# Kernel optimization log

Hardware: AMD Instinct MI355X
Metric: run time of the kernel (lower is better)

Reference implementation:

```python
import jax, jax.numpy as jnp
import numpy as np

N = 50000        # nodes
E = 800000       # edges (avg degree 16)
HIDDEN = 256
HEADS = 8
HEAD_DIM = HIDDEN // HEADS


def _linear_params(key, fan_in, fan_out):
    k1, k2 = jax.random.split(key)
    s = 1.0 / np.sqrt(fan_in)
    W = jax.random.uniform(k1, (fan_in, fan_out), jnp.float32, -s, s)
    b = jax.random.uniform(k2, (fan_out,), jnp.float32, -s, s)
    return W, b


def setup_inputs() -> dict:
    key = jax.random.key(0)
    ks = jax.random.split(key, 7)
    h = jax.random.normal(ks[0], (N, HIDDEN), jnp.float32)
    # sparse adjacency nonzeros: row = destination node, col = source node
    row = jnp.sort(jax.random.randint(ks[1], (E,), 0, N))
    col = jax.random.randint(ks[2], (E,), 0, N)
    Wq, bq = _linear_params(ks[3], HIDDEN, HIDDEN)
    Wk, bk = _linear_params(ks[4], HIDDEN, HIDDEN)
    Wv, bv = _linear_params(ks[5], HIDDEN, HIDDEN)
    Wo, bo = _linear_params(ks[6], HIDDEN, HIDDEN)
    return dict(h=h, row=row, col=col, Wq=Wq, bq=bq, Wk=Wk, bk=bk,
                Wv=Wv, bv=bv, Wo=Wo, bo=bo)


def reference(h, row, col, Wq, bq, Wk, bk, Wv, bv, Wo, bo):
    n = h.shape[0]
    scaling = HEAD_DIM ** (-0.5)
    q = ((h @ Wq + bq).reshape(n, HEADS, HEAD_DIM)) * scaling
    k = (h @ Wk + bk).reshape(n, HEADS, HEAD_DIM)
    v = (h @ Wv + bv).reshape(n, HEADS, HEAD_DIM)

    # bsddmm: per-edge, per-head sampled dot product q[dst] . k[src] -> [E, H]
    s = jnp.einsum('ehd,ehd->eh', q[row], k[col])

    # sparse row-wise softmax over each destination node's incoming edges
    m = jax.ops.segment_max(s, row, num_segments=n)          # [N, H]
    p = jnp.exp(s - m[row])                                   # [E, H]
    denom = jax.ops.segment_sum(p, row, num_segments=n)      # [N, H]
    attn = p / denom[row]                                     # [E, H]

    # bspmm: out[dst] = sum over incoming edges attn * v[src] -> [N, H, D]
    out = jax.ops.segment_sum(attn[:, :, None] * v[col], row, num_segments=n)
    return out.reshape(n, HIDDEN) @ Wo + bo
```

## Files before the change

kernel.cpp:

```cpp
#include <hip/hip_runtime.h>
#include <math.h>


typedef __attribute__((ext_vector_type(8))) short bf16x8;
typedef __attribute__((ext_vector_type(4))) float f32x4;
typedef __attribute__((ext_vector_type(2))) float f32x2;

__device__ __forceinline__ ushort f2bf(float f) {
    uint u = __float_as_uint(f);
    u += 0x7fffu + ((u >> 16) & 1u);
    return (ushort)(u >> 16);
}
__device__ __forceinline__ float bflo(uint u) { return __uint_as_float(u << 16); }
__device__ __forceinline__ float bfhi(uint u) { return __uint_as_float(u & 0xffff0000u); }

__device__ __forceinline__ uchar f2fp8(float f) {
    return (uchar)(__builtin_amdgcn_cvt_pk_fp8_f32(f, f, 0, false) & 0xff);
}
__device__ __forceinline__ void fp8x4_to_f32(uint u, float* f) {
    f32x2 lo = __builtin_amdgcn_cvt_pk_f32_fp8(u, false);
    f32x2 hi = __builtin_amdgcn_cvt_pk_f32_fp8(u, true);
    f[0] = lo[0]; f[1] = lo[1]; f[2] = hi[0]; f[3] = hi[1];
}

__device__ __forceinline__ void load_lds16(const void* g, void* l) {
    __builtin_amdgcn_global_load_lds(
        (const __attribute__((address_space(1))) void*)g,
        (__attribute__((address_space(3))) void*)l, 16, 0, 0);
}

__global__ __launch_bounds__(256) void convert_bf16(
    const float* __restrict__ in, ushort* __restrict__ out, size_t nelem)
{
    size_t i = ((size_t)blockIdx.x * 256 + threadIdx.x) * 4;
    if (i >= nelem) return;
    float4 v = *(const float4*)(in + i);
    *(ushort4*)(out + i) = make_ushort4(f2bf(v.x), f2bf(v.y), f2bf(v.z), f2bf(v.w));
}

__global__ __launch_bounds__(256) void prep(
    const float* __restrict__ Wq, const float* __restrict__ Wk,
    const float* __restrict__ Wv, const float* __restrict__ Wo,
    const float* __restrict__ bq, const float* __restrict__ bk,
    const float* __restrict__ bv,
    const int* __restrict__ row, int* __restrict__ row_ptr, int n, int E,
    ushort* __restrict__ Wall, ushort* __restrict__ Wot,
    float* __restrict__ ball)
{
    int m = blockIdx.y;
    if (m == 4) {
        int i = blockIdx.x * 256 + threadIdx.x;
        if (i > n) return;
        int lo = 0, hi = E;
        while (lo < hi) {
            int mid = (lo + hi) >> 1;
            if (row[mid] < i) lo = mid + 1; else hi = mid;
        }
        row_ptr[i] = lo;
        return;
    }
    if (blockIdx.x < 256) {
        int idx = blockIdx.x * 256 + threadIdx.x;
        int k = idx >> 8, nn = idx & 255;
        if (m < 3) {
            const float* W = m == 0 ? Wq : (m == 1 ? Wk : Wv);
            Wall[((size_t)m * 256 + nn) * 256 + k] = f2bf(W[idx]);
        } else {
            Wot[nn * 256 + k] = f2bf(Wo[idx]);
        }
    } else if (m < 3) {
        int i = threadIdx.x;
        ball[m * 256 + i] = (m == 0 ? bq : (m == 1 ? bk : bv))[i];
    }
}

template<int MODE>
__global__ __launch_bounds__(256) void gemm_mfma_lds(
    const ushort* __restrict__ A, const ushort* __restrict__ Wt,
    const float* __restrict__ bias, ushort* __restrict__ qb,
    uchar* __restrict__ kv, float* __restrict__ vscale,
    float* __restrict__ outf, int n, float scale)
{
    __shared__ ushort SH[2 * 128 * 64];
    ushort* As = SH;
    ushort* Bs = SH + 128 * 64;

    const int nwg = gridDim.x * gridDim.y;
    const int orig = blockIdx.y * gridDim.x + blockIdx.x;
    const int xcd = orig & 7, rnd = orig >> 3;
    const int q8 = nwg >> 3, r8 = nwg & 7;
    const int wgid = (xcd < r8 ? xcd * (q8 + 1) : r8 * (q8 + 1) + (xcd - r8) * q8) + rnd;
    const int tx = wgid % gridDim.x;
    const int ty = wgid / gridDim.x;

    const int tid = threadIdx.x;
    const int lane = tid & 63;
    const int wave = tid >> 6;
    const int col0 = tx * 128;
    const int row0 = ty * 128;
    const int fr = lane & 15;
    const int kg = lane >> 4;
    const int wr = (wave >> 1) * 64;
    const int wc = (wave & 1) * 64;

    f32x4 acc[4][4] = {};

    const int srow = tid >> 3;
    const int sc8 = tid & 7;

    for (int kt = 0; kt < 4; ++kt) {
        #pragma unroll
        for (int it = 0; it < 4; ++it) {
            int r = srow + it * 32;
            int chunk = sc8 ^ (r & 7);
            int ar = row0 + r; ar = ar < n ? ar : n - 1;
            load_lds16((const char*)A + (size_t)ar * 512 + kt * 128 + chunk * 16,
                       (char*)As + (it * 256 + tid) * 16);
            load_lds16((const char*)Wt + (size_t)(col0 + r) * 512 + kt * 128 + chunk * 16,
                       (char*)Bs + (it * 256 + tid) * 16);
        }
        __syncthreads();

        #pragma unroll
        for (int ks = 0; ks < 2; ++ks) {
            bf16x8 a[4], b[4];
            #pragma unroll
            for (int i = 0; i < 4; ++i) {
                int r = wr + i * 16 + fr;
                int chunk = (ks * 4 + kg) ^ (r & 7);
                a[i] = *(const bf16x8*)((const char*)As + r * 128 + chunk * 16);
            }
            #pragma unroll
            for (int j = 0; j < 4; ++j) {
                int c = wc + j * 16 + fr;
                int chunk = (ks * 4 + kg) ^ (c & 7);
                b[j] = *(const bf16x8*)((const char*)Bs + c * 128 + chunk * 16);
            }
            #pragma unroll
            for (int i = 0; i < 4; ++i)
                #pragma unroll
                for (int j = 0; j < 4; ++j)
                    acc[i][j] = __builtin_amdgcn_mfma_f32_16x16x32_bf16(
                        a[i], b[j], acc[i][j], 0, 0, 0);
        }
        __syncthreads();
    }

    if constexpr (MODE == 1) {
        #pragma unroll
        for (int j = 0; j < 4; ++j) {
            int gcol = col0 + wc + j * 16 + fr;
            float bj = bias[gcol];
            #pragma unroll
            for (int i = 0; i < 4; ++i) {
                #pragma unroll
                for (int r = 0; r < 4; ++r) {
                    int grow = row0 + wr + i * 16 + kg * 4 + r;
                    if (grow >= n) continue;
                    outf[(size_t)grow * 256 + gcol] = acc[i][j][r] + bj;
                }
            }
        }
        return;
    }

    char* sb = (char*)SH;
    const bool isf8 = (col0 >= 256 && col0 < 512);
    const bool isv  = (col0 >= 512);
    const float sc = (col0 < 256) ? scale : 1.f;

    #pragma unroll
    for (int j = 0; j < 4; ++j) {
        int cw = wc + j * 16 + fr;
        float bj = bias[col0 + cw];
        #pragma unroll
        for (int i = 0; i < 4; ++i) {
            #pragma unroll
            for (int r2 = 0; r2 < 4; ++r2) {
                int lrow = wr + i * 16 + kg * 4 + r2;
                float val = (acc[i][j][r2] + bj) * sc;
                if (isf8) {
                    int u = cw >> 4;
                    sb[lrow * 128 + ((u ^ (lrow & 7)) << 4) + (cw & 15)] = f2fp8(val);
                } else {
                    int u = cw >> 3;
                    *(ushort*)(sb + lrow * 256 + ((u ^ (lrow & 7)) << 4) +
                               ((cw & 7) << 1)) = f2bf(val);
                }
            }
        }
    }
    __syncthreads();

    if (isf8) {
        int seg = col0 - 256;
        #pragma unroll
        for (int pass = 0; pass < 4; ++pass) {
            int g = pass * 256 + tid;
            int lrow = g >> 3, u = g & 7;
            uint4 d = *(const uint4*)(sb + lrow * 128 + ((u ^ (lrow & 7)) << 4));
            int grow = row0 + lrow;
            if (grow < n)
                *(uint4*)((char*)kv + (size_t)grow * 512 + seg + u * 16) = d;
        }
    } else if (isv) {
        int vseg = col0 - 512;
        #pragma unroll
        for (int pass = 0; pass < 2; ++pass) {
            int t = pass * 256 + tid;
            int lrow = t >> 2, hh = t & 3;
            float vals[32];
            #pragma unroll
            for (int uu = 0; uu < 4; ++uu) {
                int u = hh * 4 + uu;
                uint4 d = *(const uint4*)(sb + lrow * 256 + ((u ^ (lrow & 7)) << 4));
                vals[uu*8+0] = bflo(d.x); vals[uu*8+1] = bfhi(d.x);
                vals[uu*8+2] = bflo(d.y); vals[uu*8+3] = bfhi(d.y);
                vals[uu*8+4] = bflo(d.z); vals[uu*8+5] = bfhi(d.z);
                vals[uu*8+6] = bflo(d.w); vals[uu*8+7] = bfhi(d.w);
            }
            float mx = 0.f;
            #pragma unroll
            for (int i = 0; i < 32; ++i) mx = fmaxf(mx, fabsf(vals[i]));
            float inv = mx > 0.f ? 127.f / mx : 0.f;
            float scl = mx > 0.f ? mx * (1.f / 127.f) : 0.f;
            uint pk[8];
            #pragma unroll
            for (int w = 0; w < 8; ++w) {
                uint b0 = (uint)(__float2int_rn(vals[w*4+0] * inv) + 128);
                uint b1 = (uint)(__float2int_rn(vals[w*4+1] * inv) + 128);
                uint b2 = (uint)(__float2int_rn(vals[w*4+2] * inv) + 128);
                uint b3 = (uint)(__float2int_rn(vals[w*4+3] * inv) + 128);
                pk[w] = b0 | (b1 << 8) | (b2 << 16) | (b3 << 24);
            }
            int grow = row0 + lrow;
            if (grow < n) {
                char* dst = (char*)kv + (size_t)grow * 512 + 256 + vseg + hh * 32;
                *(uint4*)dst        = make_uint4(pk[0], pk[1], pk[2], pk[3]);
                *(uint4*)(dst + 16) = make_uint4(pk[4], pk[5], pk[6], pk[7]);
                vscale[(size_t)grow * 8 + (vseg >> 5) + hh] = scl;
            }
        }
    } else {
        #pragma unroll
        for (int pass = 0; pass < 8; ++pass) {
            int g = pass * 256 + tid;
            int lrow = g >> 4, u = g & 15;
            uint4 d = *(const uint4*)(sb + lrow * 256 + ((u ^ (lrow & 7)) << 4));
            int grow = row0 + lrow;
            if (grow < n)
                *(uint4*)((char*)qb + (size_t)grow * 512 + col0 * 2 + u * 16) = d;
        }
    }
}

__global__ __launch_bounds__(256) void fused_attn(
    const ushort* __restrict__ qb, const uchar* __restrict__ kv,
    const float* __restrict__ vscale, const int* __restrict__ col,
    const int* __restrict__ row_ptr, ushort* __restrict__ agg, int n)
{
    int node = blockIdx.x * 4 + (threadIdx.x >> 6);
    if (node >= n) return;
    int lane = threadIdx.x & 63;
    int p0 = row_ptr[node], p1 = row_ptr[node + 1];

    const int slot = lane >> 4;
    const int l16 = lane & 15;
    const int qoff = l16 * 32;

    float qf[16];
    {
        const char* qbp = (const char*)qb + (size_t)node * 512 + qoff;
        uint4 q0 = *(const uint4*)qbp;
        uint4 q1 = *(const uint4*)(qbp + 16);
        qf[0] = bflo(q0.x); qf[1] = bfhi(q0.x);
        qf[2] = bflo(q0.y); qf[3] = bfhi(q0.y);
        qf[4] = bflo(q0.z); qf[5] = bfhi(q0.z);
        qf[6] = bflo(q0.w); qf[7] = bfhi(q0.w);
        qf[8] = bflo(q1.x); qf[9] = bfhi(q1.x);
        qf[10] = bflo(q1.y); qf[11] = bfhi(q1.y);
        qf[12] = bflo(q1.z); qf[13] = bfhi(q1.z);
        qf[14] = bflo(q1.w); qf[15] = bfhi(q1.w);
    }

    float denom = 0.f;
    float cacc = 0.f;
    float acc[16] = {};

#define ISSUE(IDX, K, V, S)                                                    \
    do {                                                                       \
        int src_ = __shfl(cl, (IDX));                                          \
        const char* b_ = (const char*)kv + (size_t)src_ * 512;                 \
        K = *(const uint4*)(b_ + l16 * 16);                                    \
        V = *(const uint4*)(b_ + 256 + l16 * 16);                              \
        S = vscale[(size_t)src_ * 8 + (l16 >> 1)];                             \
    } while (0)

#define CONSUME(VALID, K, V, S)                                                \
    do {                                                                       \
        float kf_[16];                                                         \
        fp8x4_to_f32(K.x, kf_); fp8x4_to_f32(K.y, kf_ + 4);                    \
        fp8x4_to_f32(K.z, kf_ + 8); fp8x4_to_f32(K.w, kf_ + 12);               \
        float sp_ = 0.f;                                                       \
        _Pragma("unroll")                                                      \
        for (int i_ = 0; i_ < 16; ++i_) sp_ = fmaf(qf[i_], kf_[i_], sp_);      \
        float s_ = sp_ + __shfl_xor(sp_, 1);                                   \
        float p_ = (VALID) ? __expf(s_) : 0.f;                                 \
        denom += p_;                                                           \
        float ps_ = p_ * (S);                                                  \
        cacc += ps_;                                                           \
        uint w_;                                                               \
        w_ = V.x;                                                              \
        acc[0]  = fmaf(ps_, (float)(w_ & 0xff),         acc[0]);               \
        acc[1]  = fmaf(ps_, (float)((w_ >> 8) & 0xff),  acc[1]);               \
        acc[2]  = fmaf(ps_, (float)((w_ >> 16) & 0xff), acc[2]);               \
        acc[3]  = fmaf(ps_, (float)(w_ >> 24),          acc[3]);               \
        w_ = V.y;                                                              \
        acc[4]  = fmaf(ps_, (float)(w_ & 0xff),         acc[4]);               \
        acc[5]  = fmaf(ps_, (float)((w_ >> 8) & 0xff),  acc[5]);               \
        acc[6]  = fmaf(ps_, (float)((w_ >> 16) & 0xff), acc[6]);               \
        acc[7]  = fmaf(ps_, (float)(w_ >> 24),          acc[7]);               \
        w_ = V.z;                                                              \
        acc[8]  = fmaf(ps_, (float)(w_ & 0xff),         acc[8]);               \
        acc[9]  = fmaf(ps_, (float)((w_ >> 8) & 0xff),  acc[9]);               \
        acc[10] = fmaf(ps_, (float)((w_ >> 16) & 0xff), acc[10]);              \
        acc[11] = fmaf(ps_, (float)(w_ >> 24),          acc[11]);              \
        w_ = V.w;                                                              \
        acc[12] = fmaf(ps_, (float)(w_ & 0xff),         acc[12]);              \
        acc[13] = fmaf(ps_, (float)((w_ >> 8) & 0xff),  acc[13]);              \
        acc[14] = fmaf(ps_, (float)((w_ >> 16) & 0xff), acc[14]);              \
        acc[15] = fmaf(ps_, (float)(w_ >> 24),          acc[15]);              \
    } while (0)

    for (int bbase = p0; bbase < p1; bbase += 64) {
        int bd = min(64, p1 - bbase);
        int cl = (lane < bd) ? col[bbase + lane] : 0;
        int nch = (bd + 3) >> 2;

        uint4 kA, vA, kB, vB; float sA, sB;
        ISSUE(slot, kA, vA, sA);
        int c = 0;
        for (;;) {
            if (c + 1 < nch) ISSUE((c + 1) * 4 + slot, kB, vB, sB);
            CONSUME(c * 4 + slot < bd, kA, vA, sA);
            if (++c >= nch) break;
            if (c + 1 < nch) ISSUE((c + 1) * 4 + slot, kA, vA, sA);
            CONSUME(c * 4 + slot < bd, kB, vB, sB);
            if (++c >= nch) break;
        }
    }
#undef ISSUE
#undef CONSUME

    #pragma unroll
    for (int i = 0; i < 16; ++i) acc[i] = fmaf(-128.f, cacc, acc[i]);
    #pragma unroll
    for (int i = 0; i < 16; ++i) {
        acc[i] += __shfl_xor(acc[i], 16);
        acc[i] += __shfl_xor(acc[i], 32);
    }
    denom += __shfl_xor(denom, 16);
    denom += __shfl_xor(denom, 32);

    if (slot == 0) {
        float inv = denom > 0.f ? 1.f / denom : 0.f;
        uint o[8];
        #pragma unroll
        for (int i = 0; i < 8; ++i)
            o[i] = (uint)f2bf(acc[2 * i] * inv) |
                   ((uint)f2bf(acc[2 * i + 1] * inv) << 16);
        char* ob = (char*)agg + (size_t)node * 512 + qoff;
        *(uint4*)ob        = make_uint4(o[0], o[1], o[2], o[3]);
        *(uint4*)(ob + 16) = make_uint4(o[4], o[5], o[6], o[7]);
    }
}

extern "C" void kernel_launch(void* const* d_in, const int* in_sizes, int n_in,
                              void* d_out, int out_size, void* d_ws, size_t ws_size,
                              hipStream_t stream)
{
    const float* h  = (const float*)d_in[0];
    const int*   row = (const int*)d_in[1];
    const int*   col = (const int*)d_in[2];
    const float* Wq = (const float*)d_in[3];
    const float* bq = (const float*)d_in[4];
    const float* Wk = (const float*)d_in[5];
    const float* bk = (const float*)d_in[6];
    const float* Wv = (const float*)d_in[7];
    const float* bv = (const float*)d_in[8];
    const float* Wo = (const float*)d_in[9];
    const float* bo = (const float*)d_in[10];
    float* out = (float*)d_out;

    const int n = in_sizes[0] / 256;
    const int E = in_sizes[1];
    const size_t NC = (size_t)n * 256;

    char* base = (char*)d_ws;
    ushort* qbb    = (ushort*)(base);
    uchar*  kv     = (uchar*)(base + NC * 2);
    float*  vscale = (float*)(base + NC * 4);
    ushort* aggb   = (ushort*)(base + NC * 4 + (size_t)n * 32);
    ushort* hb     = (ushort*)(base + NC * 6 + (size_t)n * 32);
    ushort* Wall   = (ushort*)(base + NC * 8 + (size_t)n * 32);
    ushort* Wot    = Wall + 768 * 256;
    float*  ball   = (float*)(Wot + 65536);
    int* row_ptr   = (int*)(ball + 768);

    const float scaling = 0.17677669529663687f;

    dim3 blk(256);
    prep<<<dim3(257, 5), blk, 0, stream>>>(Wq, Wk, Wv, Wo, bq, bk, bv,
                                           row, row_ptr, n, E,
                                           Wall, Wot, ball);
    convert_bf16<<<dim3((int)((NC / 4 + 255) / 256)), blk, 0, stream>>>(h, hb, NC);

    const int mtiles = (n + 127) / 128;
    gemm_mfma_lds<0><<<dim3(6, mtiles), blk, 0, stream>>>(
        hb, Wall, ball, qbb, kv, vscale, nullptr, n, scaling);

    fused_attn<<<dim3((n + 3) / 4), blk, 0, stream>>>(
        qbb, kv, vscale, col, row_ptr, aggb, n);

    gemm_mfma_lds<1><<<dim3(2, mtiles), blk, 0, stream>>>(
        aggb, Wot, bo, nullptr, nullptr, nullptr, out, n, 1.f);
}
```

Before: 156.9 us.

## Quantize Q and K to int8 and compute attention scores with sdot4

Q is now stored as per-head int8 with a per-head scale, and K as int8 with one scale per 128-column half, replacing bf16 Q and fp8 K. The score dot product then uses packed int8 dot instructions instead of fp8 unpacking and float FMAs, and the per-node Q read shrinks by half. This cuts conversion ALU work and memory traffic in the attention kernel. The cost is an extra scale load per edge, coarser K quantization (scale shared across four heads), and more quantization work in the GEMM epilogue.

```diff
diff --git a/kernel.cpp b/kernel.cpp
--- a/kernel.cpp
+++ b/kernel.cpp
@@ -4,7 +4,6 @@
 
 typedef __attribute__((ext_vector_type(8))) short bf16x8;
 typedef __attribute__((ext_vector_type(4))) float f32x4;
-typedef __attribute__((ext_vector_type(2))) float f32x2;
 
 __device__ __forceinline__ ushort f2bf(float f) {
     uint u = __float_as_uint(f);
@@ -14,14 +13,18 @@
 __device__ __forceinline__ float bflo(uint u) { return __uint_as_float(u << 16); }
 __device__ __forceinline__ float bfhi(uint u) { return __uint_as_float(u & 0xffff0000u); }
 
-__device__ __forceinline__ uchar f2fp8(float f) {
-    return (uchar)(__builtin_amdgcn_cvt_pk_fp8_f32(f, f, 0, false) & 0xff);
-}
-__device__ __forceinline__ void fp8x4_to_f32(uint u, float* f) {
-    f32x2 lo = __builtin_amdgcn_cvt_pk_f32_fp8(u, false);
-    f32x2 hi = __builtin_amdgcn_cvt_pk_f32_fp8(u, true);
-    f[0] = lo[0]; f[1] = lo[1]; f[2] = hi[0]; f[3] = hi[1];
-}
+#if __has_builtin(__builtin_amdgcn_sdot4)
+__device__ __forceinline__ int SDOT4(uint a, uint b, int c) {
+    return __builtin_amdgcn_sdot4((int)a, (int)b, c, false);
+}
+#else
+__device__ __forceinline__ int SDOT4(uint a, uint b, int c) {
+    #pragma unroll
+    for (int i = 0; i < 4; ++i)
+        c += ((int)(a << (24 - 8 * i)) >> 24) * ((int)(b << (24 - 8 * i)) >> 24);
+    return c;
+}
+#endif
 
 __device__ __forceinline__ void load_lds16(const void* g, void* l) {
     __builtin_amdgcn_global_load_lds(
@@ -77,8 +80,9 @@
 template<int MODE>
 __global__ __launch_bounds__(256) void gemm_mfma_lds(
     const ushort* __restrict__ A, const ushort* __restrict__ Wt,
-    const float* __restrict__ bias, ushort* __restrict__ qb,
-    uchar* __restrict__ kv, float* __restrict__ vscale,
+    const float* __restrict__ bias, char* __restrict__ qb8,
+    float* __restrict__ qscale, uchar* __restrict__ kv,
+    float* __restrict__ kscale, float* __restrict__ vscale,
     float* __restrict__ outf, int n, float scale)
 {
     __shared__ ushort SH[2 * 128 * 64];
@@ -165,8 +169,6 @@
     }
 
     char* sb = (char*)SH;
-    const bool isf8 = (col0 >= 256 && col0 < 512);
-    const bool isv  = (col0 >= 512);
     const float sc = (col0 < 256) ? scale : 1.f;
 
     #pragma unroll
@@ -179,32 +181,58 @@
             for (int r2 = 0; r2 < 4; ++r2) {
                 int lrow = wr + i * 16 + kg * 4 + r2;
                 float val = (acc[i][j][r2] + bj) * sc;
-                if (isf8) {
-                    int u = cw >> 4;
-                    sb[lrow * 128 + ((u ^ (lrow & 7)) << 4) + (cw & 15)] = f2fp8(val);
-                } else {
-                    int u = cw >> 3;
-                    *(ushort*)(sb + lrow * 256 + ((u ^ (lrow & 7)) << 4) +
-                               ((cw & 7) << 1)) = f2bf(val);
-                }
+                int u = cw >> 3;
+                *(ushort*)(sb + lrow * 256 + ((u ^ (lrow & 7)) << 4) +
+                           ((cw & 7) << 1)) = f2bf(val);
             }
         }
     }
     __syncthreads();
 
-    if (isf8) {
-        int seg = col0 - 256;
-        #pragma unroll
-        for (int pass = 0; pass < 4; ++pass) {
-            int g = pass * 256 + tid;
-            int lrow = g >> 3, u = g & 7;
-            uint4 d = *(const uint4*)(sb + lrow * 128 + ((u ^ (lrow & 7)) << 4));
+    if (col0 >= 256 && col0 < 512) {
+        int kseg = col0 - 256;
+        int khalf = kseg >> 7;
+        #pragma unroll
+        for (int pass = 0; pass < 2; ++pass) {
+            int t = pass * 256 + tid;
+            int lrow = t >> 2, sub = t & 3;
+            float vals[32];
+            #pragma unroll
+            for (int uu = 0; uu < 4; ++uu) {
+                int u = sub * 4 + uu;
+                uint4 d = *(const uint4*)(sb + lrow * 256 + ((u ^ (lrow & 7)) << 4));
+                vals[uu*8+0] = bflo(d.x); vals[uu*8+1] = bfhi(d.x);
+                vals[uu*8+2] = bflo(d.y); vals[uu*8+3] = bfhi(d.y);
+                vals[uu*8+4] = bflo(d.z); vals[uu*8+5] = bfhi(d.z);
+                vals[uu*8+6] = bflo(d.w); vals[uu*8+7] = bfhi(d.w);
+            }
+            float mx = 0.f;
+            #pragma unroll
+            for (int i = 0; i < 32; ++i) mx = fmaxf(mx, fabsf(vals[i]));
+            mx = fmaxf(mx, __shfl_xor(mx, 1));
+            mx = fmaxf(mx, __shfl_xor(mx, 2));
+            float inv = mx > 0.f ? 127.f / mx : 0.f;
+            float scl = mx > 0.f ? mx * (1.f / 127.f) : 0.f;
+            uint pk[8];
+            #pragma unroll
+            for (int w = 0; w < 8; ++w) {
+                uint b0 = (uint)__float2int_rn(vals[w*4+0] * inv) & 0xff;
+                uint b1 = (uint)__float2int_rn(vals[w*4+1] * inv) & 0xff;
+                uint b2 = (uint)__float2int_rn(vals[w*4+2] * inv) & 0xff;
+                uint b3 = (uint)__float2int_rn(vals[w*4+3] * inv) & 0xff;
+                pk[w] = b0 | (b1 << 8) | (b2 << 16) | (b3 << 24);
+            }
             int grow = row0 + lrow;
-            if (grow < n)
-                *(uint4*)((char*)kv + (size_t)grow * 512 + seg + u * 16) = d;
-        }
-    } else if (isv) {
-        int vseg = col0 - 512;
+            if (grow < n) {
+                char* dst = (char*)kv + (size_t)grow * 512 + kseg + sub * 32;
+                *(uint4*)dst        = make_uint4(pk[0], pk[1], pk[2], pk[3]);
+                *(uint4*)(dst + 16) = make_uint4(pk[4], pk[5], pk[6], pk[7]);
+                if (sub == 0) kscale[(size_t)grow * 2 + khalf] = scl;
+            }
+        }
+    } else {
+        const bool isq = (col0 < 256);
+        int seg = isq ? col0 : (col0 - 512);
         #pragma unroll
         for (int pass = 0; pass < 2; ++pass) {
             int t = pass * 256 + tid;
@@ -227,35 +255,30 @@
             uint pk[8];
             #pragma unroll
             for (int w = 0; w < 8; ++w) {
-                uint b0 = (uint)(__float2int_rn(vals[w*4+0] * inv) + 128);
-                uint b1 = (uint)(__float2int_rn(vals[w*4+1] * inv) + 128);
-                uint b2 = (uint)(__float2int_rn(vals[w*4+2] * inv) + 128);
-                uint b3 = (uint)(__float2int_rn(vals[w*4+3] * inv) + 128);
-                pk[w] = b0 | (b1 << 8) | (b2 << 16) | (b3 << 24);
+                int b0 = __float2int_rn(vals[w*4+0] * inv);
+                int b1 = __float2int_rn(vals[w*4+1] * inv);
+                int b2 = __float2int_rn(vals[w*4+2] * inv);
+                int b3 = __float2int_rn(vals[w*4+3] * inv);
+                if (!isq) { b0 += 128; b1 += 128; b2 += 128; b3 += 128; }
+                pk[w] = ((uint)b0 & 0xff) | (((uint)b1 & 0xff) << 8) |
+                        (((uint)b2 & 0xff) << 16) | (((uint)b3 & 0xff) << 24);
             }
             int grow = row0 + lrow;
             if (grow < n) {
-                char* dst = (char*)kv + (size_t)grow * 512 + 256 + vseg + hh * 32;
+                char* dst = isq ? (qb8 + (size_t)grow * 256 + seg + hh * 32)
+                                : ((char*)kv + (size_t)grow * 512 + 256 + seg + hh * 32);
                 *(uint4*)dst        = make_uint4(pk[0], pk[1], pk[2], pk[3]);
                 *(uint4*)(dst + 16) = make_uint4(pk[4], pk[5], pk[6], pk[7]);
-                vscale[(size_t)grow * 8 + (vseg >> 5) + hh] = scl;
-            }
-        }
-    } else {
-        #pragma unroll
-        for (int pass = 0; pass < 8; ++pass) {
-            int g = pass * 256 + tid;
-            int lrow = g >> 4, u = g & 15;
-            uint4 d = *(const uint4*)(sb + lrow * 256 + ((u ^ (lrow & 7)) << 4));
-            int grow = row0 + lrow;
-            if (grow < n)
-                *(uint4*)((char*)qb + (size_t)grow * 512 + col0 * 2 + u * 16) = d;
+                float* sdst = isq ? qscale : vscale;
+                sdst[(size_t)grow * 8 + (seg >> 5) + hh] = scl;
+            }
         }
     }
 }
 
 __global__ __launch_bounds__(256) void fused_attn(
-    const ushort* __restrict__ qb, const uchar* __restrict__ kv,
+    const char* __restrict__ qb8, const float* __restrict__ qscale,
+    const uchar* __restrict__ kv, const float* __restrict__ kscale,
     const float* __restrict__ vscale, const int* __restrict__ col,
     const int* __restrict__ row_ptr, ushort* __restrict__ agg, int n)
 {
@@ -266,48 +289,36 @@
 
     const int slot = lane >> 4;
     const int l16 = lane & 15;
-    const int qoff = l16 * 32;
-
-    float qf[16];
-    {
-        const char* qbp = (const char*)qb + (size_t)node * 512 + qoff;
-        uint4 q0 = *(const uint4*)qbp;
-        uint4 q1 = *(const uint4*)(qbp + 16);
-        qf[0] = bflo(q0.x); qf[1] = bfhi(q0.x);
-        qf[2] = bflo(q0.y); qf[3] = bfhi(q0.y);
-        qf[4] = bflo(q0.z); qf[5] = bfhi(q0.z);
-        qf[6] = bflo(q0.w); qf[7] = bfhi(q0.w);
-        qf[8] = bflo(q1.x); qf[9] = bfhi(q1.x);
-        qf[10] = bflo(q1.y); qf[11] = bfhi(q1.y);
-        qf[12] = bflo(q1.z); qf[13] = bfhi(q1.z);
-        qf[14] = bflo(q1.w); qf[15] = bfhi(q1.w);
-    }
+    const int aoff = l16 * 32;
+
+    uint4 qi = *(const uint4*)(qb8 + (size_t)node * 256 + l16 * 16);
+    float qs = qscale[(size_t)node * 8 + (l16 >> 1)];
 
     float denom = 0.f;
     float cacc = 0.f;
     float acc[16] = {};
 
-#define ISSUE(IDX, K, V, S)                                                    \
+#define ISSUE(IDX, K, V, KS, VS)                                               \
     do {                                                                       \
         int src_ = __shfl(cl, (IDX));                                          \
         const char* b_ = (const char*)kv + (size_t)src_ * 512;                 \
         K = *(const uint4*)(b_ + l16 * 16);                                    \
         V = *(const uint4*)(b_ + 256 + l16 * 16);                              \
-        S = vscale[(size_t)src_ * 8 + (l16 >> 1)];                             \
+        KS = kscale[(size_t)src_ * 2 + (l16 >> 3)];                            \
+        VS = vscale[(size_t)src_ * 8 + (l16 >> 1)];                            \
     } while (0)
 
-#define CONSUME(VALID, K, V, S)                                                \
+#define CONSUME(VALID, K, V, KS, VS)                                           \
     do {                                                                       \
-        float kf_[16];                                                         \
-        fp8x4_to_f32(K.x, kf_); fp8x4_to_f32(K.y, kf_ + 4);                    \
-        fp8x4_to_f32(K.z, kf_ + 8); fp8x4_to_f32(K.w, kf_ + 12);               \
-        float sp_ = 0.f;                                                       \
-        _Pragma("unroll")                                                      \
-        for (int i_ = 0; i_ < 16; ++i_) sp_ = fmaf(qf[i_], kf_[i_], sp_);      \
-        float s_ = sp_ + __shfl_xor(sp_, 1);                                   \
+        int id_ = SDOT4(qi.x, K.x, 0);                                         \
+        id_ = SDOT4(qi.y, K.y, id_);                                           \
+        id_ = SDOT4(qi.z, K.z, id_);                                           \
+        id_ = SDOT4(qi.w, K.w, id_);                                           \
+        int it_ = id_ + __shfl_xor(id_, 1);                                    \
+        float s_ = (float)it_ * (qs * (KS));                                   \
         float p_ = (VALID) ? __expf(s_) : 0.f;                                 \
         denom += p_;                                                           \
-        float ps_ = p_ * (S);                                                  \
+        float ps_ = p_ * (VS);                                                 \
         cacc += ps_;                                                           \
         uint w_;                                                               \
         w_ = V.x;                                                              \
@@ -337,15 +348,15 @@
         int cl = (lane < bd) ? col[bbase + lane] : 0;
         int nch = (bd + 3) >> 2;
 
-        uint4 kA, vA, kB, vB; float sA, sB;
-        ISSUE(slot, kA, vA, sA);
+        uint4 kA, vA, kB, vB; float ksA, vsA, ksB, vsB;
+        ISSUE(slot, kA, vA, ksA, vsA);
         int c = 0;
         for (;;) {
-            if (c + 1 < nch) ISSUE((c + 1) * 4 + slot, kB, vB, sB);
-            CONSUME(c * 4 + slot < bd, kA, vA, sA);
+            if (c + 1 < nch) ISSUE((c + 1) * 4 + slot, kB, vB, ksB, vsB);
+            CONSUME(c * 4 + slot < bd, kA, vA, ksA, vsA);
             if (++c >= nch) break;
-            if (c + 1 < nch) ISSUE((c + 1) * 4 + slot, kA, vA, sA);
-            CONSUME(c * 4 + slot < bd, kB, vB, sB);
+            if (c + 1 < nch) ISSUE((c + 1) * 4 + slot, kA, vA, ksA, vsA);
+            CONSUME(c * 4 + slot < bd, kB, vB, ksB, vsB);
             if (++c >= nch) break;
         }
     }
@@ -369,7 +380,7 @@
         for (int i = 0; i < 8; ++i)
             o[i] = (uint)f2bf(acc[2 * i] * inv) |
                    ((uint)f2bf(acc[2 * i + 1] * inv) << 16);
-        char* ob = (char*)agg + (size_t)node * 512 + qoff;
+        char* ob = (char*)agg + (size_t)node * 512 + aoff;
         *(uint4*)ob        = make_uint4(o[0], o[1], o[2], o[3]);
         *(uint4*)(ob + 16) = make_uint4(o[4], o[5], o[6], o[7]);
     }
@@ -397,12 +408,14 @@
     const size_t NC = (size_t)n * 256;
 
     char* base = (char*)d_ws;
-    ushort* qbb    = (ushort*)(base);
-    uchar*  kv     = (uchar*)(base + NC * 2);
-    float*  vscale = (float*)(base + NC * 4);
-    ushort* aggb   = (ushort*)(base + NC * 4 + (size_t)n * 32);
-    ushort* hb     = (ushort*)(base + NC * 6 + (size_t)n * 32);
-    ushort* Wall   = (ushort*)(base + NC * 8 + (size_t)n * 32);
+    char*   qb8    = base;
+    uchar*  kv     = (uchar*)(base + (size_t)n * 256);
+    float*  qscale = (float*)(base + (size_t)n * 768);
+    float*  vscale = (float*)(base + (size_t)n * 800);
+    float*  kscale = (float*)(base + (size_t)n * 832);
+    ushort* aggb   = (ushort*)(base + (size_t)n * 840);
+    ushort* hb     = (ushort*)(base + (size_t)n * 1352);
+    ushort* Wall   = (ushort*)(base + (size_t)n * 1864);
     ushort* Wot    = Wall + 768 * 256;
     float*  ball   = (float*)(Wot + 65536);
     int* row_ptr   = (int*)(ball + 768);
@@ -417,11 +430,11 @@
 
     const int mtiles = (n + 127) / 128;
     gemm_mfma_lds<0><<<dim3(6, mtiles), blk, 0, stream>>>(
-        hb, Wall, ball, qbb, kv, vscale, nullptr, n, scaling);
+        hb, Wall, ball, qb8, qscale, kv, kscale, vscale, nullptr, n, scaling);
 
     fused_attn<<<dim3((n + 3) / 4), blk, 0, stream>>>(
-        qbb, kv, vscale, col, row_ptr, aggb, n);
+        qb8, qscale, kv, kscale, vscale, col, row_ptr, aggb, n);
 
     gemm_mfma_lds<1><<<dim3(2, mtiles), blk, 0, stream>>>(
-        aggb, Wot, bo, nullptr, nullptr, nullptr, out, n, 1.f);
-}
+        aggb, Wot, bo, nullptr, nullptr, nullptr, nullptr, nullptr, out, n, 1.f);
+}
```

Measured after the change: 155.6 us (median of 2 runs). No clear change (-0.8%).
